# Kernel tuning notes

Hardware: AMD Instinct MI355X
Metric: run time of the kernel (lower is better)

## Reference

```python
import jax, jax.numpy as jnp
import numpy as np
from jax import lax

B = 16384
NWIRES = 4


def _conv(x, w, b):
    # NCHW conv, stride 1, SAME padding (pad 1 for k=3)
    y = lax.conv_general_dilated(x, w, (1, 1), ((1, 1), (1, 1)),
                                 dimension_numbers=("NCHW", "OIHW", "NCHW"))
    return y + b[None, :, None, None]


def _pool2(x):
    b, c, h, w = x.shape
    return x.reshape(b, c, h // 2, 2, w // 2, 2).max(axis=(3, 5))


def _apply_1q(state, U, wire):
    # state: (B,2,2,2,2) complex; U: (B,2,2) complex
    s = jnp.moveaxis(state, wire + 1, -1)
    s = jnp.einsum("bij,b...j->b...i", U, s)
    return jnp.moveaxis(s, -1, wire + 1)


def _apply_cnot(state, c, t):
    s0 = jnp.take(state, 0, axis=c + 1)
    s1 = jnp.take(state, 1, axis=c + 1)
    ta = t + 1 if t < c else t  # target axis index after removing control axis
    s1 = jnp.flip(s1, axis=ta)
    return jnp.stack([s0, s1], axis=c + 1)


def _ry(th):
    c = jnp.cos(th / 2)
    s = jnp.sin(th / 2)
    U = jnp.stack([jnp.stack([c, -s], -1), jnp.stack([s, c], -1)], -2)
    return U.astype(jnp.complex64)


def _rz(th):
    e = jnp.exp(-0.5j * th.astype(jnp.complex64))
    z = jnp.zeros_like(e)
    return jnp.stack([jnp.stack([e, z], -1), jnp.stack([z, jnp.conj(e)], -1)], -2)


def _rx(th):
    c = jnp.cos(th / 2).astype(jnp.complex64)
    s = jnp.sin(th / 2).astype(jnp.complex64)
    return jnp.stack([jnp.stack([c, -1j * s], -1), jnp.stack([-1j * s, c], -1)], -2)


def _circuit(params):
    # params: (B, 16) -> PauliZ expvals (B, 4)
    b = params.shape[0]
    state = jnp.zeros((b, 16), jnp.complex64).at[:, 0].set(1.0).reshape(b, 2, 2, 2, 2)
    for i in range(NWIRES):
        state = _apply_1q(state, _ry(params[:, 4 * i + 0]), i)
        state = _apply_1q(state, _rz(params[:, 4 * i + 1]), i)
        state = _apply_1q(state, _rx(params[:, 4 * i + 2]), i)
        state = _apply_cnot(state, i, (i + 1) % NWIRES)
    probs = state.real ** 2 + state.imag ** 2  # (B,2,2,2,2)
    zs = []
    for i in range(NWIRES):
        p = probs.sum(axis=tuple(a for a in range(1, 5) if a != i + 1))  # (B,2)
        zs.append(p[:, 0] - p[:, 1])
    return jnp.stack(zs, axis=-1)


def setup_inputs() -> dict:
    key = jax.random.key(0)
    ks = jax.random.split(key, 12)
    d = {}
    d["x"] = jax.random.normal(ks[0], (B, 1, 28, 28), jnp.float32)
    d["conv1_w"] = jax.random.normal(ks[1], (4, 1, 3, 3), jnp.float32) * 0.3
    d["conv1_b"] = jax.random.normal(ks[2], (4,), jnp.float32) * 0.1
    d["conv2_w"] = jax.random.normal(ks[3], (4, 4, 3, 3), jnp.float32) * 0.15
    d["conv2_b"] = jax.random.normal(ks[4], (4,), jnp.float32) * 0.1
    d["pl_w"] = jax.random.normal(ks[5], (16, 196), jnp.float32) * 0.07
    d["pl_b"] = jax.random.normal(ks[6], (16,), jnp.float32) * 0.05
    d["ro_w"] = jax.random.normal(ks[7], (4, 4), jnp.float32) * 0.5
    d["ro_b"] = jax.random.normal(ks[8], (4,), jnp.float32) * 0.1
    d["bn_w"] = jnp.ones((4,), jnp.float32)
    d["bn_b"] = jnp.zeros((4,), jnp.float32)
    return d


def reference(x, conv1_w, conv1_b, conv2_w, conv2_b, pl_w, pl_b, ro_w, ro_b, bn_w, bn_b):
    h = _pool2(jax.nn.relu(_conv(x, conv1_w, conv1_b)))   # (B,4,14,14)
    h = _pool2(jax.nn.relu(_conv(h, conv2_w, conv2_b)))   # (B,4,7,7)
    flat = h.reshape(x.shape[0], -1)                      # (B,196)
    params = flat @ pl_w.T + pl_b                         # (B,16)
    z = _circuit(params)                                  # (B,4)
    out = z @ ro_w.T + ro_b                               # (B,4)
    mean = out.mean(0)
    var = out.var(0)  # biased, matches torch BN training normalization
    return (out - mean) / jnp.sqrt(var + 1e-5) * bn_w + bn_b
```

## Files before the change

kernel.cpp:

```cpp
#include <hip/hip_runtime.h>
#include <math.h>

#define BATCH 16384

typedef float v2f __attribute__((ext_vector_type(2)));
typedef unsigned short u16;
typedef __attribute__((ext_vector_type(8))) short short8;
typedef __attribute__((ext_vector_type(4))) float f32x4;

__device__ __forceinline__ v2f pk_fma(v2f a, v2f b, v2f c) {
  return __builtin_elementwise_fma(a, b, c);
}
__device__ __forceinline__ v2f pk_max(v2f a, v2f b) {
  return __builtin_elementwise_max(a, b);
}

__device__ __forceinline__ unsigned bf2(float lo, float hi) {
  unsigned a = __float_as_uint(lo);
  unsigned b = __float_as_uint(hi);
  a = (a + 0x7fffu + ((a >> 16) & 1u)) >> 16;
  b = (b + 0x7fffu + ((b >> 16) & 1u)) & 0xffff0000u;
  return a | b;
}

__device__ __forceinline__ unsigned cvtpk(float lo, float hi) {
  unsigned r;
  asm("v_cvt_pk_bf16_f32 %0, %1, %2" : "=v"(r) : "v"(lo), "v"(hi));
  return r;
}

__global__ __launch_bounds__(256) void qnat_fused(
    const float* __restrict__ x,
    const float* __restrict__ w1,
    const float* __restrict__ b1,
    const float* __restrict__ w2,
    const float* __restrict__ b2,
    const float* __restrict__ plw,
    const float* __restrict__ plb,
    const float* __restrict__ rw,
    const float* __restrict__ rb,
    float* __restrict__ pre,
    float* __restrict__ stats)
{
  __shared__ __align__(16) float h1p[4][4 * 288 + 16];
  __shared__ __align__(16) u16 h2b[16][232];
  __shared__ __align__(16) uint4 plw_tb[28 * 16];
  __shared__ float s_red[4][8];

  const int tid = threadIdx.x;
  const int w = tid >> 6;
  const int lane = tid & 63;
  const int base = (blockIdx.x * 4 + w) * 4;

  #pragma unroll
  for (int j = 0; j < 2; j++) {
    int s = tid + 256 * j;
    if (s < 448) {
      int tp = s >> 4;
      int k2 = s & 15;
      uint4 v = make_uint4(0u, 0u, 0u, 0u);
      if (tp < 25) {
        const float4* pr = (const float4*)(plw + k2 * 196);
        float4 a = pr[2 * tp];
        float4 b = (tp < 24) ? pr[2 * tp + 1] : make_float4(0.f, 0.f, 0.f, 0.f);
        v = make_uint4(bf2(a.x, a.y), bf2(a.z, a.w),
                       bf2(b.x, b.y), bf2(b.z, b.w));
      }
      plw_tb[s] = v;
    }
  }

  {
    float4 z4 = make_float4(0.f, 0.f, 0.f, 0.f);
    float4* hz = (float4*)&h1p[w][0];
    #pragma unroll
    for (int t = 0; t < 5; t++) {
      int p = t * 64 + lane;
      if (p < 292) hz[p] = z4;
    }
    uint4 z4u = make_uint4(0u, 0u, 0u, 0u);
    uint4* hz2 = (uint4*)h2b;
    #pragma unroll
    for (int t = 0; t < 2; t++) {
      int p = tid + 256 * t;
      if (p < 464) hz2[p] = z4u;
    }
  }
  __syncthreads();

  const int i = lane >> 2;
  const int q = lane & 3;
  const bool c1act = lane < 56;

  float4 pfa[4], pfb[4];
  float pe0[4], pe1[4];
  #pragma unroll
  for (int r = 0; r < 4; r++) {
    pfa[r] = make_float4(0,0,0,0); pfb[r] = make_float4(0,0,0,0);
    pe0[r] = 0.0f; pe1[r] = 0.0f;
  }

  if (c1act) {
    const float* xb = x + (size_t)base * 784;
    #pragma unroll
    for (int r = 0; r < 4; r++) {
      int row = 2 * i - 1 + r;
      if (0 <= row && row < 28) {
        const float* rp = xb + row * 28;
        pfa[r] = *(const float4*)(rp + 8 * q);
        if (q > 0) pe0[r] = rp[8 * q - 1];
        if (q < 3) {
          pfb[r] = *(const float4*)(rp + 8 * q + 4);
          pe1[r] = rp[8 * q + 8];
        }
      }
    }
  }

  #pragma unroll 1
  for (int it = 0; it < 4; ++it) {
    if (c1act) {
      float win[4][10];
      #pragma unroll
      for (int r = 0; r < 4; r++) {
        win[r][0] = pe0[r];
        win[r][1] = pfa[r].x; win[r][2] = pfa[r].y;
        win[r][3] = pfa[r].z; win[r][4] = pfa[r].w;
        win[r][5] = pfb[r].x; win[r][6] = pfb[r].y;
        win[r][7] = pfb[r].z; win[r][8] = pfb[r].w;
        win[r][9] = pe1[r];
      }
      if (it != 3) {
        const float* xn = x + (size_t)(base + it + 1) * 784;
        #pragma unroll
        for (int r = 0; r < 4; r++) {
          int row = 2 * i - 1 + r;
          pfa[r] = make_float4(0,0,0,0);
          pfb[r] = make_float4(0,0,0,0);
          pe0[r] = 0.0f; pe1[r] = 0.0f;
          if (0 <= row && row < 28) {
            const float* rp = xn + row * 28;
            pfa[r] = *(const float4*)(rp + 8 * q);
            if (q > 0) pe0[r] = rp[8 * q - 1];
            if (q < 3) {
              pfb[r] = *(const float4*)(rp + 8 * q + 4);
              pe1[r] = rp[8 * q + 8];
            }
          }
        }
      }
      v2f P[4][9];
      #pragma unroll
      for (int r = 0; r < 4; r++)
        #pragma unroll
        for (int k = 0; k < 9; k++) P[r][k] = (v2f){win[r][k], win[r][k + 1]};

      float* hb = &h1p[w][18 * (i + 1) + 1 + 4 * q];
      #pragma unroll
      for (int c = 0; c < 4; c++) {
        const float* wc = w1 + c * 9;
        const v2f bias2 = (v2f){b1[c], b1[c]};
        v2f a0[4], a1[4];
        #pragma unroll
        for (int jj = 0; jj < 4; jj++) { a0[jj] = bias2; a1[jj] = bias2; }
        #pragma unroll
        for (int dy = 0; dy < 3; dy++)
          #pragma unroll
          for (int dx = 0; dx < 3; dx++) {
            const float wv = wc[dy * 3 + dx];
            const v2f wvv = (v2f){wv, wv};
            #pragma unroll
            for (int jj = 0; jj < 4; jj++) {
              a0[jj] = pk_fma(P[dy][2 * jj + dx],     wvv, a0[jj]);
              a1[jj] = pk_fma(P[dy + 1][2 * jj + dx], wvv, a1[jj]);
            }
          }
        float m[4];
        #pragma unroll
        for (int jj = 0; jj < 4; jj++) {
          v2f mm = pk_max(a0[jj], a1[jj]);
          m[jj] = fmaxf(fmaxf(mm.x, mm.y), 0.0f);
        }
        float* p = hb + 288 * c;
        if (q < 3) {
          p[0] = m[0];
          *(float2*)(p + 1) = make_float2(m[1], m[2]);
          p[3] = m[3];
        } else {
          p[0] = m[0];
          p[1] = m[1];
        }
      }
    }

    {
      const int jq = lane & 7;
      const int i2 = lane >> 3;
      if (i2 < 7 && jq < 7) {
        v2f acc[4][2];
        #pragma unroll
        for (int co = 0; co < 4; co++) {
          const v2f bb = (v2f){b2[co], b2[co]};
          acc[co][0] = bb; acc[co][1] = bb;
        }
        #pragma unroll
        for (int ci = 0; ci < 4; ci++) {
          const float* rp = &h1p[w][288 * ci + 36 * i2 + 2 * jq];
          v2f Q[4][3];
          #pragma unroll
          for (int r = 0; r < 4; r++) {
            v2f a = *(const v2f*)(rp + 18 * r);
            v2f b = *(const v2f*)(rp + 18 * r + 2);
            Q[r][0] = a;
            Q[r][1] = (v2f){a.y, b.x};
            Q[r][2] = b;
          }
          #pragma unroll
          for (int co = 0; co < 4; co++) {
            const float* wp = w2 + (co * 4 + ci) * 9;
            #pragma unroll
            for (int dy = 0; dy < 3; dy++)
              #pragma unroll
              for (int dx = 0; dx < 3; dx++) {
                const float wv = wp[dy * 3 + dx];
                const v2f wvv = (v2f){wv, wv};
                acc[co][0] = pk_fma(Q[dy][dx],     wvv, acc[co][0]);
                acc[co][1] = pk_fma(Q[dy + 1][dx], wvv, acc[co][1]);
              }
          }
        }
        float mo[4];
        #pragma unroll
        for (int co = 0; co < 4; co++) {
          v2f mm = pk_max(acc[co][0], acc[co][1]);
          mo[co] = fmaxf(fmaxf(mm.x, mm.y), 0.0f);
        }
        unsigned u01 = cvtpk(mo[0], mo[1]);
        unsigned u23 = cvtpk(mo[2], mo[3]);
        u16* hp = &h2b[w * 4 + it][7 * i2 + jq];
        hp[0]   = (u16)u01;
        hp[49]  = (u16)(u01 >> 16);
        hp[98]  = (u16)u23;
        hp[147] = (u16)(u23 >> 16);
      }
    }
  }
  __syncthreads();

  const int s2 = lane >> 4;
  const int k = lane & 15;

  float cv, sv;
  {
    const int arow = lane & 15;
    const int kg = lane >> 4;
    const short8* ha = (const short8*)&h2b[arow][0];
    const short8* hbw = (const short8*)plw_tb;
    f32x4 acc = {0.f, 0.f, 0.f, 0.f};
    #pragma unroll
    for (int kt = 0; kt < 7; kt++) {
      short8 av = ha[4 * kt + kg];
      short8 bv = hbw[(4 * kt + kg) * 16 + arow];
      acc = __builtin_amdgcn_mfma_f32_16x16x32_bf16(av, bv, acc, 0, 0, 0);
    }
    const int srcl = 16 * w + k;
    float c0 = __shfl(acc[0], srcl, 64);
    float c1 = __shfl(acc[1], srcl, 64);
    float c2 = __shfl(acc[2], srcl, 64);
    float c3 = __shfl(acc[3], srcl, 64);
    float pv = (s2 & 2) ? ((s2 & 1) ? c3 : c2) : ((s2 & 1) ? c1 : c0);
    pv += plb[k];
    __sincosf(pv * 0.5f, &sv, &cv);
  }

  {
    const int l = k;
    const int gb = lane & 48;
    float re = (l == 0) ? 1.0f : 0.0f;
    float im = 0.0f;
    #pragma unroll
    for (int qi = 0; qi < 4; qi++) {
      const int beta = 3 - qi;
      const int m = 1 << beta;
      const int b = (l >> beta) & 1;
      float c = __shfl(cv, gb + 4 * qi, 64), s = __shfl(sv, gb + 4 * qi, 64);
      float pr_ = __shfl_xor(re, m, 64), pi_ = __shfl_xor(im, m, 64);
      float sg = b ? s : -s;
      re = fmaf(c, re, sg * pr_);
      im = fmaf(c, im, sg * pi_);
      c = __shfl(cv, gb + 4 * qi + 1, 64); s = __shfl(sv, gb + 4 * qi + 1, 64);
      float sz = b ? s : -s;
      float nr = c * re - sz * im;
      float ni = c * im + sz * re;
      re = nr; im = ni;
      c = __shfl(cv, gb + 4 * qi + 2, 64); s = __shfl(sv, gb + 4 * qi + 2, 64);
      pr_ = __shfl_xor(re, m, 64); pi_ = __shfl_xor(im, m, 64);
      nr = fmaf(c, re, s * pi_);
      ni = fmaf(c, im, -s * pr_);
      re = nr; im = ni;
      const int tm = 1 << (3 - ((qi + 1) & 3));
      float fr = __shfl_xor(re, tm, 64), fi = __shfl_xor(im, tm, 64);
      if (b) { re = fr; im = fi; }
    }
    float pr2 = re * re + im * im;
    float z0 = ((l >> 3) & 1) ? -pr2 : pr2;
    float z1 = ((l >> 2) & 1) ? -pr2 : pr2;
    float z2 = ((l >> 1) & 1) ? -pr2 : pr2;
    float z3 = (l & 1) ? -pr2 : pr2;
    #pragma unroll
    for (int off = 8; off >= 1; off >>= 1) {
      z0 += __shfl_xor(z0, off, 64);
      z1 += __shfl_xor(z1, off, 64);
      z2 += __shfl_xor(z2, off, 64);
      z3 += __shfl_xor(z3, off, 64);
    }
    float as0 = 0.f, as1 = 0.f, as2 = 0.f, as3 = 0.f;
    float aq0 = 0.f, aq1 = 0.f, aq2 = 0.f, aq3 = 0.f;
    if (l == 0) {
      float o0 = fmaf(rw[0],  z0, fmaf(rw[1],  z1, fmaf(rw[2],  z2, fmaf(rw[3],  z3, rb[0]))));
      float o1 = fmaf(rw[4],  z0, fmaf(rw[5],  z1, fmaf(rw[6],  z2, fmaf(rw[7],  z3, rb[1]))));
      float o2 = fmaf(rw[8],  z0, fmaf(rw[9],  z1, fmaf(rw[10], z2, fmaf(rw[11], z3, rb[2]))));
      float o3 = fmaf(rw[12], z0, fmaf(rw[13], z1, fmaf(rw[14], z2, fmaf(rw[15], z3, rb[3]))));
      *(float4*)(pre + (size_t)(base + s2) * 4) = make_float4(o0, o1, o2, o3);
      as0 = o0; aq0 = o0 * o0;
      as1 = o1; aq1 = o1 * o1;
      as2 = o2; aq2 = o2 * o2;
      as3 = o3; aq3 = o3 * o3;
    }
    #pragma unroll
    for (int off = 32; off >= 16; off >>= 1) {
      as0 += __shfl_down(as0, off, 64); aq0 += __shfl_down(aq0, off, 64);
      as1 += __shfl_down(as1, off, 64); aq1 += __shfl_down(aq1, off, 64);
      as2 += __shfl_down(as2, off, 64); aq2 += __shfl_down(aq2, off, 64);
      as3 += __shfl_down(as3, off, 64); aq3 += __shfl_down(aq3, off, 64);
    }
    if (lane == 0) {
      s_red[w][0] = as0; s_red[w][4] = aq0;
      s_red[w][1] = as1; s_red[w][5] = aq1;
      s_red[w][2] = as2; s_red[w][6] = aq2;
      s_red[w][3] = as3; s_red[w][7] = aq3;
    }
  }
  __syncthreads();
  if (tid < 8) {
    float v = s_red[0][tid] + s_red[1][tid] + s_red[2][tid] + s_red[3][tid];
    atomicAdd(&stats[tid], v);
  }
}

__global__ __launch_bounds__(256) void qnat_bn(
    float* __restrict__ pre,
    const float* __restrict__ stats,
    const float* __restrict__ bnw,
    const float* __restrict__ bnb)
{
  int idx = blockIdx.x * 256 + threadIdx.x;
  int c = idx & 3;
  float mean = stats[c] * (1.0f / BATCH);
  float ex2 = stats[4 + c] * (1.0f / BATCH);
  float var = ex2 - mean * mean;
  float inv = rsqrtf(var + 1e-5f);
  pre[idx] = (pre[idx] - mean) * inv * bnw[c] + bnb[c];
}

extern "C" void kernel_launch(void* const* d_in, const int* in_sizes, int n_in,
                              void* d_out, int out_size, void* d_ws, size_t ws_size,
                              hipStream_t stream) {
  const float* x   = (const float*)d_in[0];
  const float* w1  = (const float*)d_in[1];
  const float* b1  = (const float*)d_in[2];
  const float* w2  = (const float*)d_in[3];
  const float* b2  = (const float*)d_in[4];
  const float* plw = (const float*)d_in[5];
  const float* plb = (const float*)d_in[6];
  const float* rw  = (const float*)d_in[7];
  const float* rb  = (const float*)d_in[8];
  const float* bnw = (const float*)d_in[9];
  const float* bnb = (const float*)d_in[10];

  float* out   = (float*)d_out;
  float* stats = (float*)d_ws;

  hipMemsetAsync(stats, 0, 8 * sizeof(float), stream);
  qnat_fused<<<BATCH / 16, 256, 0, stream>>>(x, w1, b1, w2, b2, plw, plb, rw, rb, out, stats);
  qnat_bn<<<(BATCH * 4) / 256, 256, 0, stream>>>(out, stats, bnw, bnb);
}
```

Before: 132.6 us.

## Compute conv2 with bf16 MFMA using pooled-window im2col weight layout

Conv1 output is now stored as bf16 in a padded shared layout indexed across all 16 samples, and conv2+maxpool is computed with 16x16x32 bf16 MFMA instructions. The weights are rearranged into a 4x4 receptive-field matrix covering the 2x2 pool window. A block-wide barrier is added between conv1 and conv2, and the pool max is taken via lane shuffles. This replaces the packed-FMA scalar conv2 with matrix cores, at the cost of bf16 precision on the intermediate activations and an extra sync.

```diff
diff --git a/kernel.cpp b/kernel.cpp
--- a/kernel.cpp
+++ b/kernel.cpp
@@ -42,9 +42,10 @@
     float* __restrict__ pre,
     float* __restrict__ stats)
 {
-  __shared__ __align__(16) float h1p[4][4 * 288 + 16];
+  __shared__ __align__(16) unsigned h1sh[16 * 513];
   __shared__ __align__(16) u16 h2b[16][232];
   __shared__ __align__(16) uint4 plw_tb[28 * 16];
+  __shared__ __align__(16) u16 b2f[64 * 16];
   __shared__ float s_red[4][8];
 
   const int tid = threadIdx.x;
@@ -70,20 +71,32 @@
     }
   }
 
+  #pragma unroll
+  for (int j = 0; j < 4; j++) {
+    int e = tid + 256 * j;
+    int kk = e >> 4, n = e & 15;
+    int ci = kk >> 4, dy = (kk >> 2) & 3, dx = kk & 3;
+    int co = n >> 2, sy = (n >> 1) & 1, sx = n & 1;
+    int ry = dy - sy, rx = dx - sx;
+    float v = 0.0f;
+    if (ry >= 0 && ry < 3 && rx >= 0 && rx < 3)
+      v = w2[((co * 4 + ci) * 3 + ry) * 3 + rx];
+    b2f[e] = (u16)bf2(v, 0.0f);
+  }
+
   {
-    float4 z4 = make_float4(0.f, 0.f, 0.f, 0.f);
-    float4* hz = (float4*)&h1p[w][0];
-    #pragma unroll
-    for (int t = 0; t < 5; t++) {
-      int p = t * 64 + lane;
-      if (p < 292) hz[p] = z4;
-    }
-    uint4 z4u = make_uint4(0u, 0u, 0u, 0u);
+    uint4 z4 = make_uint4(0u, 0u, 0u, 0u);
+    uint4* hz = (uint4*)h1sh;
+    #pragma unroll
+    for (int t = 0; t < 9; t++) {
+      int p = tid + 256 * t;
+      if (p < 2052) hz[p] = z4;
+    }
     uint4* hz2 = (uint4*)h2b;
     #pragma unroll
     for (int t = 0; t < 2; t++) {
       int p = tid + 256 * t;
-      if (p < 464) hz2[p] = z4u;
+      if (p < 464) hz2[p] = z4;
     }
   }
   __syncthreads();
@@ -155,7 +168,7 @@
         #pragma unroll
         for (int k = 0; k < 9; k++) P[r][k] = (v2f){win[r][k], win[r][k + 1]};
 
-      float* hb = &h1p[w][18 * (i + 1) + 1 + 4 * q];
+      u16* hs = (u16*)h1sh + (4 * w + it) * 1026 + (i + 1) * 16 + 4 * q;
       #pragma unroll
       for (int c = 0; c < 4; c++) {
         const float* wc = w1 + c * 9;
@@ -181,67 +194,71 @@
           v2f mm = pk_max(a0[jj], a1[jj]);
           m[jj] = fmaxf(fmaxf(mm.x, mm.y), 0.0f);
         }
-        float* p = hb + 288 * c;
+        u16* p = hs + c * 256;
+        p[1] = (u16)cvtpk(m[0], m[0]);
         if (q < 3) {
-          p[0] = m[0];
-          *(float2*)(p + 1) = make_float2(m[1], m[2]);
-          p[3] = m[3];
+          *(unsigned*)(p + 2) = cvtpk(m[1], m[2]);
+          p[4] = (u16)cvtpk(m[3], m[3]);
         } else {
-          p[0] = m[0];
-          p[1] = m[1];
-        }
-      }
-    }
-
-    {
-      const int jq = lane & 7;
-      const int i2 = lane >> 3;
-      if (i2 < 7 && jq < 7) {
-        v2f acc[4][2];
-        #pragma unroll
-        for (int co = 0; co < 4; co++) {
-          const v2f bb = (v2f){b2[co], b2[co]};
-          acc[co][0] = bb; acc[co][1] = bb;
-        }
-        #pragma unroll
-        for (int ci = 0; ci < 4; ci++) {
-          const float* rp = &h1p[w][288 * ci + 36 * i2 + 2 * jq];
-          v2f Q[4][3];
-          #pragma unroll
-          for (int r = 0; r < 4; r++) {
-            v2f a = *(const v2f*)(rp + 18 * r);
-            v2f b = *(const v2f*)(rp + 18 * r + 2);
-            Q[r][0] = a;
-            Q[r][1] = (v2f){a.y, b.x};
-            Q[r][2] = b;
-          }
-          #pragma unroll
-          for (int co = 0; co < 4; co++) {
-            const float* wp = w2 + (co * 4 + ci) * 9;
-            #pragma unroll
-            for (int dy = 0; dy < 3; dy++)
-              #pragma unroll
-              for (int dx = 0; dx < 3; dx++) {
-                const float wv = wp[dy * 3 + dx];
-                const v2f wvv = (v2f){wv, wv};
-                acc[co][0] = pk_fma(Q[dy][dx],     wvv, acc[co][0]);
-                acc[co][1] = pk_fma(Q[dy + 1][dx], wvv, acc[co][1]);
-              }
-          }
-        }
-        float mo[4];
-        #pragma unroll
-        for (int co = 0; co < 4; co++) {
-          v2f mm = pk_max(acc[co][0], acc[co][1]);
-          mo[co] = fmaxf(fmaxf(mm.x, mm.y), 0.0f);
-        }
-        unsigned u01 = cvtpk(mo[0], mo[1]);
-        unsigned u23 = cvtpk(mo[2], mo[3]);
-        u16* hp = &h2b[w * 4 + it][7 * i2 + jq];
-        hp[0]   = (u16)u01;
-        hp[49]  = (u16)(u01 >> 16);
-        hp[98]  = (u16)u23;
-        hp[147] = (u16)(u23 >> 16);
+          p[2] = (u16)cvtpk(m[1], m[1]);
+        }
+      }
+    }
+  }
+  __syncthreads();
+
+  {
+    const int n = lane & 15;
+    const int g = lane >> 4;
+    short8 bfr0, bfr1;
+    #pragma unroll
+    for (int j = 0; j < 8; j++) {
+      bfr0[j] = (short)b2f[(8 * g + j) * 16 + n];
+      bfr1[j] = (short)b2f[(32 + 8 * g + j) * 16 + n];
+    }
+    const float b2v = b2[n >> 2];
+    const int ci0 = g >> 1;
+    const int dy0 = 2 * (g & 1);
+    const int dbase = n * 513 + ci0 * 128 + dy0 * 8;
+    const unsigned* hp = h1sh;
+
+    #pragma unroll 2
+    for (int t = 0; t < 13; t++) {
+      int p = 4 * t + w;
+      if (p < 49) {
+        int i2 = (p * 9363) >> 16;
+        int j2 = p - 7 * i2;
+        int d = dbase + i2 * 16 + j2;
+        f32x4 acc = {0.f, 0.f, 0.f, 0.f};
+        {
+          unsigned A0 = hp[d],       A1 = hp[d + 1];
+          unsigned A2 = hp[d + 8],   A3 = hp[d + 9];
+          short8 av = __builtin_bit_cast(short8, make_uint4(A0, A1, A2, A3));
+          acc = __builtin_amdgcn_mfma_f32_16x16x32_bf16(av, bfr0, acc, 0, 0, 0);
+        }
+        {
+          unsigned A0 = hp[d + 256], A1 = hp[d + 257];
+          unsigned A2 = hp[d + 264], A3 = hp[d + 265];
+          short8 av = __builtin_bit_cast(short8, make_uint4(A0, A1, A2, A3));
+          acc = __builtin_amdgcn_mfma_f32_16x16x32_bf16(av, bfr1, acc, 0, 0, 0);
+        }
+        float r0 = acc[0], r1 = acc[1], r2 = acc[2], r3 = acc[3];
+        r0 = fmaxf(r0, __shfl_xor(r0, 1, 64)); r0 = fmaxf(r0, __shfl_xor(r0, 2, 64));
+        r1 = fmaxf(r1, __shfl_xor(r1, 1, 64)); r1 = fmaxf(r1, __shfl_xor(r1, 2, 64));
+        r2 = fmaxf(r2, __shfl_xor(r2, 1, 64)); r2 = fmaxf(r2, __shfl_xor(r2, 2, 64));
+        r3 = fmaxf(r3, __shfl_xor(r3, 1, 64)); r3 = fmaxf(r3, __shfl_xor(r3, 2, 64));
+        if ((lane & 3) == 0) {
+          int co = n >> 2;
+          u16* hq = &h2b[4 * g][49 * co + p];
+          float v0 = fmaxf(r0 + b2v, 0.0f);
+          float v1 = fmaxf(r1 + b2v, 0.0f);
+          float v2 = fmaxf(r2 + b2v, 0.0f);
+          float v3 = fmaxf(r3 + b2v, 0.0f);
+          hq[0]       = (u16)cvtpk(v0, v0);
+          hq[232]     = (u16)cvtpk(v1, v1);
+          hq[464]     = (u16)cvtpk(v2, v2);
+          hq[696]     = (u16)cvtpk(v3, v3);
+        }
       }
     }
   }
```

Result: no change. 130.1 us (median of 2 runs) (-1.9%).
